# Kernel tuning notes

Hardware: AMD Instinct MI355X
Metric: run time of the kernel (lower is better)

Reference implementation:

```python
import jax, jax.numpy as jnp
import numpy as np

B, S, D_IN, D_K, D_OUT = 8, 2048, 1024, 64, 64

def setup_inputs() -> dict:
    key = jax.random.key(0)
    k1, k2, k3, k4 = jax.random.split(key, 4)
    sc = 1.0 / np.sqrt(D_IN)
    return {
        "X": jax.random.normal(k1, (B, S, D_IN), dtype=jnp.float32),
        "Wq": jax.random.normal(k2, (D_IN, D_K), dtype=jnp.float32) * sc,
        "Wk": jax.random.normal(k3, (D_IN, D_K), dtype=jnp.float32) * sc,
        "Wv": jax.random.normal(k4, (D_IN, D_OUT), dtype=jnp.float32) * sc,
    }

def reference(X, Wq, Wk, Wv):
    # projections (no bias)
    Q = jnp.einsum('bsd,dk->bsk', X, Wq)   # [B,S,d_k]
    K = jnp.einsum('bsd,dk->bsk', X, Wk)   # [B,S,d_k]
    V = jnp.einsum('bsd,dv->bsv', X, Wv)   # [B,S,d_out]
    d_k = Q.shape[-1]
    S_mat = jnp.einsum('bqk,bsk->bqs', Q, K) / jnp.sqrt(jnp.float32(d_k))
    # causal mask: positions j > i get -inf
    causal = jnp.tril(jnp.ones((X.shape[1], X.shape[1]), dtype=bool))
    S_mat = jnp.where(causal[None, :, :], S_mat, -jnp.inf)
    A = jax.nn.softmax(S_mat, axis=-1)
    return jnp.einsum('bqs,bsv->bqv', A, V)
```

## Files before the change

kernel.cpp:

```cpp
#include <hip/hip_runtime.h>
#include <hip/hip_bf16.h>
#include <cstdint>
#include <cstddef>

#define BATCH 8
#define SEQ   2048
#define DIN   1024

typedef float f32x4 __attribute__((ext_vector_type(4)));
typedef float f32x8 __attribute__((ext_vector_type(8)));
typedef __bf16 bf16x8 __attribute__((ext_vector_type(8)));
typedef unsigned short ushort8_t __attribute__((ext_vector_type(8)));

__device__ __forceinline__ unsigned short bfu(float f) {
  __bf16 h = (__bf16)f;
  return __builtin_bit_cast(unsigned short, h);
}

__device__ __forceinline__ bf16x8 cvt8pair(float4 a, float4 b) {
  f32x8 v;
  v[0] = a.x; v[1] = a.y; v[2] = a.z; v[3] = a.w;
  v[4] = b.x; v[5] = b.y; v[6] = b.z; v[7] = b.w;
  return __builtin_convertvector(v, bf16x8);
}

__global__ void pack_w(const float* __restrict__ Wq, const float* __restrict__ Wk,
                       const float* __restrict__ Wv, unsigned short* __restrict__ Wp) {
  const int t = blockIdx.x * blockDim.x + threadIdx.x;
  const int lane = t & 63;
  const int grp = t >> 6;
  const int ks = grp & 31;
  const int nt = grp >> 5;
  const int n = nt * 16 + (lane & 15);
  const int k0 = ks * 32 + ((lane >> 4) << 3);
  const float* W;
  int col;
  float scale = 1.0f;
  if (n < 64)       { W = Wq; col = n;       scale = 0.125f; }
  else if (n < 128) { W = Wk; col = n - 64;  }
  else              { W = Wv; col = n - 128; }
  ushort8_t out;
#pragma unroll
  for (int j = 0; j < 8; ++j)
    out[j] = bfu(W[(size_t)(k0 + j) * 64 + col] * scale);
  reinterpret_cast<ushort8_t*>(Wp)[t] = out;
}

__global__ __launch_bounds__(256) void qkv_gemm(
    const float* __restrict__ X, const unsigned short* __restrict__ Wp,
    unsigned short* __restrict__ Qb, unsigned short* __restrict__ Kb,
    unsigned short* __restrict__ Vt) {
  __shared__ ushort8_t Af[2048];

  const int tid = threadIdx.x;
  const int lane = tid & 63;
  const int wave = tid >> 6;
  const int l15 = lane & 15;
  const int quad = lane >> 4;
  const int m0 = blockIdx.x * 32;
  const int nt0 = wave * 3;

  const int sr = tid >> 3;
  const int sk = tid & 7;
  const float* xrow = X + (size_t)(m0 + sr) * DIN;

  const ushort8_t* wp = reinterpret_cast<const ushort8_t*>(Wp) + nt0 * 2048 + lane;
  ushort8_t breg[2][3];
#pragma unroll
  for (int p = 0; p < 2; ++p)
#pragma unroll
    for (int nt = 0; nt < 3; ++nt) breg[p][nt] = wp[p * 64 + nt * 2048];

  f32x4 acc[2][3];
#pragma unroll
  for (int mt = 0; mt < 2; ++mt)
#pragma unroll
    for (int nt = 0; nt < 3; ++nt) acc[mt][nt] = (f32x4){0.f, 0.f, 0.f, 0.f};

  for (int half = 0; half < 2; ++half) {
    const int ksbase = half * 16;
    if (half) __syncthreads();
#pragma unroll
    for (int p = 0; p < 2; ++p) {
      const int ksl = sk + p * 8;
      const float4* src =
          reinterpret_cast<const float4*>(xrow + (ksbase + ksl) * 32);
      float4 f[8];
#pragma unroll
      for (int i = 0; i < 8; ++i) f[i] = src[i];
#pragma unroll
      for (int q = 0; q < 4; ++q)
        Af[(ksl * 4 + q) * 32 + sr] =
            __builtin_bit_cast(ushort8_t, cvt8pair(f[q * 2], f[q * 2 + 1]));
    }
    __syncthreads();

    for (int ksl = 0; ksl < 16; ++ksl) {
      const int ks = ksbase + ksl;
      const int p = ks & 1;
      bf16x8 af0 = __builtin_bit_cast(bf16x8, Af[(ksl * 4 + quad) * 32 + l15]);
      bf16x8 af1 = __builtin_bit_cast(bf16x8, Af[(ksl * 4 + quad) * 32 + 16 + l15]);
      bf16x8 b0 = __builtin_bit_cast(bf16x8, breg[p][0]);
      bf16x8 b1 = __builtin_bit_cast(bf16x8, breg[p][1]);
      bf16x8 b2 = __builtin_bit_cast(bf16x8, breg[p][2]);
      if (ks < 30) {
#pragma unroll
        for (int nt = 0; nt < 3; ++nt)
          breg[p][nt] = wp[(ks + 2) * 64 + nt * 2048];
      }
      acc[0][0] = __builtin_amdgcn_mfma_f32_16x16x32_bf16(af0, b0, acc[0][0], 0, 0, 0);
      acc[0][1] = __builtin_amdgcn_mfma_f32_16x16x32_bf16(af0, b1, acc[0][1], 0, 0, 0);
      acc[0][2] = __builtin_amdgcn_mfma_f32_16x16x32_bf16(af0, b2, acc[0][2], 0, 0, 0);
      acc[1][0] = __builtin_amdgcn_mfma_f32_16x16x32_bf16(af1, b0, acc[1][0], 0, 0, 0);
      acc[1][1] = __builtin_amdgcn_mfma_f32_16x16x32_bf16(af1, b1, acc[1][1], 0, 0, 0);
      acc[1][2] = __builtin_amdgcn_mfma_f32_16x16x32_bf16(af1, b2, acc[1][2], 0, 0, 0);
    }
  }

#pragma unroll
  for (int mt = 0; mt < 2; ++mt) {
    const int srow = m0 + mt * 16 + quad * 4;
    const int b = srow >> 11;
    const int s = srow & 2047;
#pragma unroll
    for (int nt = 0; nt < 3; ++nt) {
      const f32x4 a = acc[mt][nt];
      const int n = (nt0 + nt) * 16 + l15;
      if (n < 64) {
#pragma unroll
        for (int r = 0; r < 4; ++r)
          Qb[(size_t)(srow + r) * 64 + n] = bfu(a[r]);
      } else if (n < 128) {
#pragma unroll
        for (int r = 0; r < 4; ++r)
          Kb[(size_t)(srow + r) * 64 + (n - 64)] = bfu(a[r]);
      } else {
        const int dv = n - 128;
        ushort4 t4;
        t4.x = bfu(a[0]); t4.y = bfu(a[1]);
        t4.z = bfu(a[2]); t4.w = bfu(a[3]);
        *reinterpret_cast<ushort4*>(Vt + (((size_t)(b * 64 + dv)) << 11) + s) = t4;
      }
    }
  }
}

__global__ __launch_bounds__(256) void flash_kernel(
    const unsigned short* __restrict__ Qb, const unsigned short* __restrict__ Kb,
    const unsigned short* __restrict__ Vt, float* __restrict__ Out) {
  __shared__ float Olds[4][2][16][68];
  __shared__ float Llds[4][2][16];
  __shared__ unsigned short Pf[4][2][2][512];

  const int tid = threadIdx.x;
  const int lane = tid & 63;
  const int wave = tid >> 6;
  const int l15 = lane & 15;
  const int quad = lane >> 4;

  const int g = blockIdx.x;
  const int batch = g & 7;
  const int qb = 63 - (g >> 3);
  const int q0 = qb * 32;
  const int n64 = (q0 + 95) >> 6;

  bf16x8 qf[2][2];
#pragma unroll
  for (int mt = 0; mt < 2; ++mt) {
    const ushort8_t* qp = reinterpret_cast<const ushort8_t*>(
        Qb + (size_t)(batch * SEQ + q0 + mt * 16 + l15) * 64);
    qf[mt][0] = __builtin_bit_cast(bf16x8, qp[quad]);
    qf[mt][1] = __builtin_bit_cast(bf16x8, qp[4 + quad]);
  }

  const ushort8_t* kbase = reinterpret_cast<const ushort8_t*>(
      Kb + (size_t)(batch * SEQ + l15) * 64);
  const unsigned short* vtb = Vt + ((size_t)(batch * 64) << 11);

  f32x4 o[2][4];
  float lacc[2][4];
#pragma unroll
  for (int mt = 0; mt < 2; ++mt)
#pragma unroll
    for (int i = 0; i < 4; ++i) {
      o[mt][i] = (f32x4){0.f, 0.f, 0.f, 0.f};
      lacc[mt][i] = 0.f;
    }

  ushort8_t kbuf[8];
  if (wave < n64) {
#pragma unroll
    for (int h = 0; h < 4; ++h) {
      const ushort8_t* kp = kbase + (size_t)(wave * 64 + h * 16) * 8;
      kbuf[h * 2] = kp[quad];
      kbuf[h * 2 + 1] = kp[4 + quad];
    }
  }

  for (int kt = wave; kt < n64; kt += 4) {
    const int k0 = kt * 64;
    f32x4 s[2][4];
#pragma unroll
    for (int h = 0; h < 4; ++h) {
      bf16x8 kf0 = __builtin_bit_cast(bf16x8, kbuf[h * 2]);
      bf16x8 kf1 = __builtin_bit_cast(bf16x8, kbuf[h * 2 + 1]);
#pragma unroll
      for (int mt = 0; mt < 2; ++mt) {
        f32x4 z = (f32x4){0.f, 0.f, 0.f, 0.f};
        z = __builtin_amdgcn_mfma_f32_16x16x32_bf16(qf[mt][0], kf0, z, 0, 0, 0);
        z = __builtin_amdgcn_mfma_f32_16x16x32_bf16(qf[mt][1], kf1, z, 0, 0, 0);
        s[mt][h] = z;
      }
    }
    {
      const int nk = (kt + 4 < n64) ? kt + 4 : n64 - 1;
#pragma unroll
      for (int h = 0; h < 4; ++h) {
        const ushort8_t* kp = kbase + (size_t)(nk * 64 + h * 16) * 8;
        kbuf[h * 2] = kp[quad];
        kbuf[h * 2 + 1] = kp[4 + quad];
      }
    }
    ushort8_t vbuf[8];
#pragma unroll
    for (int c = 0; c < 2; ++c)
#pragma unroll
      for (int nt = 0; nt < 4; ++nt)
        vbuf[c * 4 + nt] = reinterpret_cast<const ushort8_t*>(
            vtb + (((size_t)(nt * 16 + l15)) << 11) + k0 + c * 32)[quad];
    if (kt == n64 - 1) {
#pragma unroll
      for (int mt = 0; mt < 2; ++mt)
#pragma unroll
        for (int h = 0; h < 4; ++h) {
          const int col = k0 + h * 16 + l15;
#pragma unroll
          for (int r = 0; r < 4; ++r) {
            const int row = q0 + mt * 16 + quad * 4 + r;
            if (col > row) s[mt][h][r] = -INFINITY;
          }
        }
    }
#pragma unroll
    for (int mt = 0; mt < 2; ++mt) {
#pragma unroll
      for (int h = 0; h < 4; ++h) {
        const int c = h >> 1;
        const int lp = ((h & 1) * 2 + (l15 >> 3)) * 16 + quad * 4;
        const int j = l15 & 7;
#pragma unroll
        for (int r = 0; r < 4; ++r) {
          const float pv = __expf(s[mt][h][r]);
          lacc[mt][r] += pv;
          Pf[wave][mt][c][(lp + r) * 8 + j] = bfu(pv);
        }
      }
    }
#pragma unroll
    for (int c = 0; c < 2; ++c) {
      bf16x8 pfm[2];
#pragma unroll
      for (int mt = 0; mt < 2; ++mt)
        pfm[mt] = __builtin_bit_cast(bf16x8,
            reinterpret_cast<const ushort8_t*>(&Pf[wave][mt][c][0])[lane]);
#pragma unroll
      for (int nt = 0; nt < 4; ++nt) {
        bf16x8 vf = __builtin_bit_cast(bf16x8, vbuf[c * 4 + nt]);
#pragma unroll
        for (int mt = 0; mt < 2; ++mt)
          o[mt][nt] = __builtin_amdgcn_mfma_f32_16x16x32_bf16(pfm[mt], vf, o[mt][nt], 0, 0, 0);
      }
    }
  }

#pragma unroll
  for (int off = 1; off < 16; off <<= 1)
#pragma unroll
    for (int mt = 0; mt < 2; ++mt)
#pragma unroll
      for (int r = 0; r < 4; ++r)
        lacc[mt][r] += __shfl_xor(lacc[mt][r], off, 64);

#pragma unroll
  for (int mt = 0; mt < 2; ++mt) {
#pragma unroll
    for (int nt = 0; nt < 4; ++nt)
#pragma unroll
      for (int r = 0; r < 4; ++r)
        Olds[wave][mt][quad * 4 + r][nt * 16 + l15] = o[mt][nt][r];
    if (l15 == 0) {
#pragma unroll
      for (int r = 0; r < 4; ++r) Llds[wave][mt][quad * 4 + r] = lacc[mt][r];
    }
  }
  __syncthreads();

  const int col = tid & 63;
  const int r0 = tid >> 6;
#pragma unroll
  for (int row = r0; row < 32; row += 4) {
    const int mt = row >> 4;
    const int rr = row & 15;
    float lstar = 0.f, accv = 0.f;
#pragma unroll
    for (int w = 0; w < 4; ++w) {
      lstar += Llds[w][mt][rr];
      accv += Olds[w][mt][rr][col];
    }
    Out[(size_t)(batch * SEQ + q0 + row) * 64 + col] = accv / lstar;
  }
}

extern "C" void kernel_launch(void* const* d_in, const int* in_sizes, int n_in,
                              void* d_out, int out_size, void* d_ws, size_t ws_size,
                              hipStream_t stream) {
  const float* X  = (const float*)d_in[0];
  const float* Wq = (const float*)d_in[1];
  const float* Wk = (const float*)d_in[2];
  const float* Wv = (const float*)d_in[3];
  float* Out = (float*)d_out;

  char* ws = (char*)d_ws;
  unsigned short* Wp = (unsigned short*)ws;
  unsigned short* Qb = (unsigned short*)(ws + (400 << 10));
  unsigned short* Kb = (unsigned short*)(ws + (400 << 10) + (2 << 20));
  unsigned short* Vt = (unsigned short*)(ws + (400 << 10) + (4 << 20));

  pack_w<<<96, 256, 0, stream>>>(Wq, Wk, Wv, Wp);
  qkv_gemm<<<512, 256, 0, stream>>>(X, Wp, Qb, Kb, Vt);
  flash_kernel<<<512, 256, 0, stream>>>(Qb, Kb, Vt, Out);
}
```

Before: 139.3 us.

## Split flash attention key range across two blocks with separate merge kernel

Doubles the flash grid so each query tile's key range is split across eight wave slots in two blocks, writing partial outputs and row sums to workspace. A new merge kernel sums the partials and normalizes. This is meant to raise occupancy and parallelism on the 256-CU device, since 512 blocks leave the work unevenly spread. The cost is an extra kernel launch and about 32MB of partial-output traffic written and then read back. It appears to rely on a fixed softmax offset with no running max, as the earlier code also did.

```diff
diff --git a/kernel.cpp b/kernel.cpp
--- a/kernel.cpp
+++ b/kernel.cpp
@@ -145,11 +145,10 @@
   }
 }
 
-__global__ __launch_bounds__(256) void flash_kernel(
+__global__ __launch_bounds__(256) void flash_main(
     const unsigned short* __restrict__ Qb, const unsigned short* __restrict__ Kb,
-    const unsigned short* __restrict__ Vt, float* __restrict__ Out) {
-  __shared__ float Olds[4][2][16][68];
-  __shared__ float Llds[4][2][16];
+    const unsigned short* __restrict__ Vt, float* __restrict__ Po,
+    float* __restrict__ Pl) {
   __shared__ unsigned short Pf[4][2][2][512];
 
   const int tid = threadIdx.x;
@@ -160,9 +159,12 @@
 
   const int g = blockIdx.x;
   const int batch = g & 7;
-  const int qb = 63 - (g >> 3);
+  const int qb = 63 - ((g >> 3) & 63);
+  const int khalf = g >> 9;
   const int q0 = qb * 32;
   const int n64 = (q0 + 95) >> 6;
+  const int slot = khalf * 4 + wave;
+  const int qg = batch * 64 + qb;
 
   bf16x8 qf[2][2];
 #pragma unroll
@@ -188,16 +190,16 @@
     }
 
   ushort8_t kbuf[8];
-  if (wave < n64) {
+  if (slot < n64) {
 #pragma unroll
     for (int h = 0; h < 4; ++h) {
-      const ushort8_t* kp = kbase + (size_t)(wave * 64 + h * 16) * 8;
+      const ushort8_t* kp = kbase + (size_t)(slot * 64 + h * 16) * 8;
       kbuf[h * 2] = kp[quad];
       kbuf[h * 2 + 1] = kp[4 + quad];
     }
   }
 
-  for (int kt = wave; kt < n64; kt += 4) {
+  for (int kt = slot; kt < n64; kt += 8) {
     const int k0 = kt * 64;
     f32x4 s[2][4];
 #pragma unroll
@@ -213,7 +215,7 @@
       }
     }
     {
-      const int nk = (kt + 4 < n64) ? kt + 4 : n64 - 1;
+      const int nk = (kt + 8 < n64) ? kt + 8 : n64 - 1;
 #pragma unroll
       for (int h = 0; h < 4; ++h) {
         const ushort8_t* kp = kbase + (size_t)(nk * 64 + h * 16) * 8;
@@ -281,34 +283,43 @@
       for (int r = 0; r < 4; ++r)
         lacc[mt][r] += __shfl_xor(lacc[mt][r], off, 64);
 
-#pragma unroll
-  for (int mt = 0; mt < 2; ++mt) {
+  float* po = Po + (size_t)(qg * 8 + slot) * 2048;
+#pragma unroll
+  for (int mt = 0; mt < 2; ++mt)
 #pragma unroll
     for (int nt = 0; nt < 4; ++nt)
 #pragma unroll
       for (int r = 0; r < 4; ++r)
-        Olds[wave][mt][quad * 4 + r][nt * 16 + l15] = o[mt][nt][r];
-    if (l15 == 0) {
-#pragma unroll
-      for (int r = 0; r < 4; ++r) Llds[wave][mt][quad * 4 + r] = lacc[mt][r];
-    }
-  }
-  __syncthreads();
-
+        po[(mt * 16 + quad * 4 + r) * 64 + nt * 16 + l15] = o[mt][nt][r];
+  if (l15 == 0) {
+    float* pl = Pl + (size_t)(qg * 8 + slot) * 32;
+#pragma unroll
+    for (int mt = 0; mt < 2; ++mt)
+#pragma unroll
+      for (int r = 0; r < 4; ++r)
+        pl[mt * 16 + quad * 4 + r] = lacc[mt][r];
+  }
+}
+
+__global__ __launch_bounds__(256) void flash_merge(
+    const float* __restrict__ Po, const float* __restrict__ Pl,
+    float* __restrict__ Out) {
+  const int tid = threadIdx.x;
   const int col = tid & 63;
-  const int r0 = tid >> 6;
-#pragma unroll
-  for (int row = r0; row < 32; row += 4) {
-    const int mt = row >> 4;
-    const int rr = row & 15;
-    float lstar = 0.f, accv = 0.f;
-#pragma unroll
-    for (int w = 0; w < 4; ++w) {
-      lstar += Llds[w][mt][rr];
-      accv += Olds[w][mt][rr][col];
-    }
-    Out[(size_t)(batch * SEQ + q0 + row) * 64 + col] = accv / lstar;
-  }
+  const int rq = tid >> 6;
+  const int brow = blockIdx.x * 4 + rq;
+  const int s = brow & 2047;
+  const int qg = (brow >> 11) * 64 + (s >> 5);
+  const int row = s & 31;
+  const float* po = Po + (size_t)(qg * 8) * 2048 + row * 64 + col;
+  const float* pl = Pl + (size_t)(qg * 8) * 32 + row;
+  float acc = 0.f, l = 0.f;
+#pragma unroll
+  for (int slot = 0; slot < 8; ++slot) {
+    acc += po[(size_t)slot * 2048];
+    l += pl[slot * 32];
+  }
+  Out[(size_t)brow * 64 + col] = acc / l;
 }
 
 extern "C" void kernel_launch(void* const* d_in, const int* in_sizes, int n_in,
@@ -325,8 +336,11 @@
   unsigned short* Qb = (unsigned short*)(ws + (400 << 10));
   unsigned short* Kb = (unsigned short*)(ws + (400 << 10) + (2 << 20));
   unsigned short* Vt = (unsigned short*)(ws + (400 << 10) + (4 << 20));
+  float* Po = (float*)(ws + (8 << 20));
+  float* Pl = (float*)(ws + (44 << 20));
 
   pack_w<<<96, 256, 0, stream>>>(Wq, Wk, Wv, Wp);
   qkv_gemm<<<512, 256, 0, stream>>>(X, Wp, Qb, Kb, Vt);
-  flash_kernel<<<512, 256, 0, stream>>>(Qb, Kb, Vt, Out);
-}
+  flash_main<<<1024, 256, 0, stream>>>(Qb, Kb, Vt, Po, Pl);
+  flash_merge<<<4096, 256, 0, stream>>>(Po, Pl, Out);
+}
```

New measurement: 146.8 us. +5.4%, slower.
